# Performance work log

Hardware: AMD Instinct MI355X
Metric: run time of the kernel (lower is better)

The kernel has to match this reference:

```python
import jax, jax.numpy as jnp
import numpy as np

N_NODES = 50000
N_EDGES = 1600000
IN_F, H_F, N_C = 128, 128, 16
NEG_SLOPE = 0.2  # DGL GATConv default


def setup_inputs() -> dict:
    key = jax.random.key(0)
    ks = jax.random.split(key, 12)
    def w(k, shape, fan_in):
        return jax.random.normal(k, shape, jnp.float32) / np.float32(np.sqrt(fan_in))
    return {
        "feat": jax.random.normal(ks[0], (N_NODES, IN_F), jnp.float32),
        "src": jax.random.randint(ks[1], (N_EDGES,), 0, N_NODES, dtype=jnp.int32),
        "dst": jax.random.randint(ks[2], (N_EDGES,), 0, N_NODES, dtype=jnp.int32),
        "W1": w(ks[3], (IN_F, H_F), IN_F), "al1": w(ks[4], (H_F,), H_F), "ar1": w(ks[5], (H_F,), H_F), "b1": jnp.zeros((H_F,), jnp.float32),
        "W2": w(ks[6], (H_F, H_F), H_F), "al2": w(ks[7], (H_F,), H_F), "ar2": w(ks[8], (H_F,), H_F), "b2": jnp.zeros((H_F,), jnp.float32),
        "W3": w(ks[9], (H_F, N_C), H_F), "al3": w(ks[10], (N_C,), N_C), "ar3": w(ks[11], (N_C,), N_C), "b3": jnp.zeros((N_C,), jnp.float32),
    }


def _gat_layer(h, src, dst, W, al, ar, b):
    # DGL GATConv (1 head): ft = W h; e_ij = LeakyReLU(a_l.ft_src + a_r.ft_dst);
    # alpha = edge_softmax over incoming edges of dst; out = sum alpha * ft_src + bias
    ft = h @ W                                   # [N, out]
    el = ft @ al                                 # [N]
    er = ft @ ar                                 # [N]
    e = jax.nn.leaky_relu(el[src] + er[dst], negative_slope=NEG_SLOPE)  # [E]
    emax = jax.ops.segment_max(e, dst, num_segments=N_NODES)
    emax = jnp.where(jnp.isfinite(emax), emax, 0.0)  # guard isolated nodes
    ex = jnp.exp(e - emax[dst])                  # [E]
    esum = jax.ops.segment_sum(ex, dst, num_segments=N_NODES)  # [N]
    agg = jax.ops.segment_sum(ex[:, None] * ft[src], dst, num_segments=N_NODES)  # [N, out]
    out = agg / jnp.where(esum > 0, esum, 1.0)[:, None] + b
    return jax.nn.relu(out)


def reference(feat, src, dst, W1, al1, ar1, b1, W2, al2, ar2, b2, W3, al3, ar3, b3):
    h = _gat_layer(feat, src, dst, W1, al1, ar1, b1)
    h = _gat_layer(h, src, dst, W2, al2, ar2, b2)
    h = _gat_layer(h, src, dst, W3, al3, ar3, b3)
    return h  # [N_NODES, N_C]
```

## Files before the change

### kernel.cpp

```cpp
#include <hip/hip_runtime.h>
#include <hip/hip_bf16.h>

#define NN 50000
#define NE 1600000
#define FF 128
#define CC 16
#define NB ((NN + 63) / 64)
#define NBLK 256
#define CH ((NE + NBLK - 1) / NBLK)

using bf16 = __hip_bfloat16;
using bf16x8 = __attribute__((ext_vector_type(8))) short;
using f32x4  = __attribute__((ext_vector_type(4))) float;

static __device__ __forceinline__ float ldf(const void* p, int i, int isbf){
    return isbf ? __bfloat162float(((const bf16*)p)[i]) : ((const float*)p)[i];
}
static __device__ __forceinline__ float bflo(unsigned u){
    union{unsigned x; float f;} c; c.x = u << 16; return c.f;
}
static __device__ __forceinline__ float bfhi(unsigned u){
    union{unsigned x; float f;} c; c.x = u & 0xFFFF0000u; return c.f;
}
static __device__ __forceinline__ float rdlanef(float v, int l){
    return __int_as_float(__builtin_amdgcn_readlane(__float_as_int(v), l));
}
static __device__ __forceinline__ unsigned short f2bfu(float v){
    bf16 b = __float2bfloat16(v);
    union{bf16 b; unsigned short u;} c; c.b = b; return c.u;
}

__global__ __launch_bounds__(256) void k_prep(const unsigned short* __restrict__ featu,
                                              const void* __restrict__ W1, const void* __restrict__ W2,
                                              const void* __restrict__ W3, int* __restrict__ dflag,
                                              int* __restrict__ bcounts, unsigned short* __restrict__ wtg){
    __shared__ int cnt;
    const int t = threadIdx.x;
    if (t == 0) cnt = 0;
    __syncthreads();
    unsigned short lo = featu[2 * t];
    int e = (lo >> 7) & 0xFF;
    if (e >= 117 && e <= 137) atomicAdd(&cnt, 1);
    __syncthreads();
    const int isbf = (cnt >= 128) ? 1 : 0;
    int idx = blockIdx.x * 256 + t;
    if (idx == 0) *dflag = isbf;
    if (idx < NB) bcounts[idx] = 0;
    if (idx < 32768){
        int l = idx >> 14;
        int e2 = idx & 16383;
        int f = e2 >> 7, k = e2 & 127;
        const void* W = l ? W2 : W1;
        wtg[idx] = f2bfu(ldf(W, k * FF + f, isbf));
    } else if (idx < 34816){
        int e2 = idx - 32768;
        int f = e2 >> 7, k = e2 & 127;
        wtg[idx] = f2bfu(ldf(W3, k * CC + f, isbf));
    }
}


__global__ __launch_bounds__(256) void k_bcount(const int* __restrict__ dst, int* __restrict__ bcounts,
                                                int* __restrict__ bh){
    __shared__ int hist[NB];
    const int t = threadIdx.x, b = blockIdx.x;
    for (int i = t; i < NB; i += 256) hist[i] = 0;
    __syncthreads();
    const int beg = b * CH, end = (beg + CH < NE) ? beg + CH : NE;
    for (int i = beg + t; i < end; i += 256){
        int d = dst[i];
        if ((unsigned)d >= NN) d = 0;
        atomicAdd(&hist[d >> 6], 1);
    }
    __syncthreads();
    for (int k = t; k < NB; k += 256){
        int v = hist[k];
        bh[k * NBLK + b] = v;
        if (v) atomicAdd(&bcounts[k], v);
    }
}

__global__ __launch_bounds__(256) void k_bscan(const int* __restrict__ bcounts, int* __restrict__ bbase,
                                               int* __restrict__ rowptr){
    __shared__ int s[256];
    const int t = threadIdx.x;
    constexpr int PT = (NB + 255) / 256;
    int loc[PT];
    int sum = 0;
    #pragma unroll
    for (int i = 0; i < PT; i++){
        int idx = t * PT + i;
        int v = (idx < NB) ? bcounts[idx] : 0;
        loc[i] = sum;
        sum += v;
    }
    s[t] = sum; __syncthreads();
    for (int off = 1; off < 256; off <<= 1){
        int x = (t >= off) ? s[t - off] : 0;
        __syncthreads();
        s[t] += x;
        __syncthreads();
    }
    int base = (t > 0) ? s[t - 1] : 0;
    #pragma unroll
    for (int i = 0; i < PT; i++){
        int idx = t * PT + i;
        if (idx < NB) bbase[idx] = base + loc[i];
    }
    if (t == 255){
        bbase[NB] = s[255];
        rowptr[NN] = s[255];
    }
}

__global__ __launch_bounds__(256) void k_boffset(const int* __restrict__ bbase, int* __restrict__ bh){
    int k = blockIdx.x * 4 + (threadIdx.x >> 6);
    int lane = threadIdx.x & 63;
    if (k >= NB) return;
    int v[4];
    int s = 0;
    #pragma unroll
    for (int i = 0; i < 4; i++){
        v[i] = bh[k * NBLK + 4 * lane + i];
        s += v[i];
    }
    int tot = s;
    #pragma unroll
    for (int off = 1; off < 64; off <<= 1){
        int x = __shfl_up(s, off);
        if (lane >= off) s += x;
    }
    int run = bbase[k] + s - tot;
    #pragma unroll
    for (int i = 0; i < 4; i++){
        bh[k * NBLK + 4 * lane + i] = run;
        run += v[i];
    }
}

__global__ __launch_bounds__(256) void k_bucket(const int* __restrict__ src, const int* __restrict__ dst,
                                                const int* __restrict__ bh, unsigned* __restrict__ bpairs){
    __shared__ int cur[NB];
    const int t = threadIdx.x, b = blockIdx.x;
    for (int k = t; k < NB; k += 256) cur[k] = bh[k * NBLK + b];
    __syncthreads();
    const int beg = b * CH, end = (beg + CH < NE) ? beg + CH : NE;
    for (int i = beg + t; i < end; i += 256){
        int s = src[i];
        int d = dst[i];
        if ((unsigned)s >= NN) s = 0;
        if ((unsigned)d >= NN) d = 0;
        int p = atomicAdd(&cur[d >> 6], 1);
        if ((unsigned)p < NE) bpairs[p] = (unsigned)s | ((unsigned)(d & 63) << 16);
    }
}

__global__ __launch_bounds__(256) void k_bsort(const unsigned* __restrict__ bpairs, const int* __restrict__ bbase,
                                               int* __restrict__ rowptr, int* __restrict__ csrsrc){
    __shared__ int cnt[64];
    __shared__ int cur[64];
    const int t = threadIdx.x;
    const int b = blockIdx.x;
    const int base = bbase[b];
    const int endb = bbase[b + 1];
    if (t < 64) cnt[t] = 0;
    __syncthreads();
    for (int i = base + t; i < endb; i += 256)
        atomicAdd(&cnt[bpairs[i] >> 16], 1);
    __syncthreads();
    if (t < 64){
        int v = cnt[t];
        int inc = v;
        #pragma unroll
        for (int off = 1; off < 64; off <<= 1){
            int x = __shfl_up(inc, off);
            if (t >= off) inc += x;
        }
        int excl = inc - v;
        cur[t] = excl;
        int d = b * 64 + t;
        if (d < NN) rowptr[d] = base + excl;
    }
    __syncthreads();
    for (int i = base + t; i < endb; i += 256){
        unsigned pr = bpairs[i];
        int p = atomicAdd(&cur[pr >> 16], 1);
        csrsrc[base + p] = (int)(pr & 0xFFFFu);
    }
}


template<bool XDYN>
__global__ __launch_bounds__(256) void k_mgemm(const void* __restrict__ X, const unsigned short* __restrict__ wtg,
                                               const void* __restrict__ al, const void* __restrict__ ar,
                                               const int* __restrict__ dflag, bf16* __restrict__ ft,
                                               float* __restrict__ el, float* __restrict__ er){
    const int isbf = *dflag;
    const int t  = threadIdx.x;
    const int n0 = blockIdx.x * 64;
    const int wv = t >> 6;
    const int lane = t & 63;
    const int quad = lane >> 4;
    const int mcol = lane & 15;
    const int row = n0 + wv * 16 + mcol;
    const int rc  = (row < NN) ? row : 0;

    bf16x8 afr[4];
    if (XDYN && !isbf){
        const float* xr = (const float*)X + rc * FF + quad * 8;
        #pragma unroll
        for (int kt = 0; kt < 4; kt++){
            float4 a = *(const float4*)(xr + kt * 32);
            float4 b = *(const float4*)(xr + kt * 32 + 4);
            union { bf16x8 v; unsigned u[4]; } c;
            c.u[0] = (unsigned)f2bfu(a.x) | ((unsigned)f2bfu(a.y) << 16);
            c.u[1] = (unsigned)f2bfu(a.z) | ((unsigned)f2bfu(a.w) << 16);
            c.u[2] = (unsigned)f2bfu(b.x) | ((unsigned)f2bfu(b.y) << 16);
            c.u[3] = (unsigned)f2bfu(b.z) | ((unsigned)f2bfu(b.w) << 16);
            afr[kt] = c.v;
        }
    } else {
        const unsigned short* xr = (const unsigned short*)X + rc * FF + quad * 8;
        #pragma unroll
        for (int kt = 0; kt < 4; kt++)
            afr[kt] = *(const bf16x8*)(xr + kt * 32);
    }

    float elp[4] = {0.f,0.f,0.f,0.f}, erp[4] = {0.f,0.f,0.f,0.f};

    #pragma unroll
    for (int f = 0; f < 8; f++){
        f32x4 acc = {0.f, 0.f, 0.f, 0.f};
        const unsigned short* wr = wtg + (f * 16 + mcol) * FF + quad * 8;
        #pragma unroll
        for (int kt = 0; kt < 4; kt++){
            bf16x8 bfr = *(const bf16x8*)(wr + kt * 32);
            acc = __builtin_amdgcn_mfma_f32_16x16x32_bf16(afr[kt], bfr, acc, 0, 0, 0);
        }
        int col = f * 16 + mcol;
        float alv = ldf(al, col, isbf);
        float arv = ldf(ar, col, isbf);
        #pragma unroll
        for (int reg = 0; reg < 4; reg++){
            int node = n0 + wv * 16 + quad * 4 + reg;
            float v = acc[reg];
            if (node < NN) ft[node * FF + col] = __float2bfloat16(v);
            elp[reg] += v * alv;
            erp[reg] += v * arv;
        }
    }

    #pragma unroll
    for (int reg = 0; reg < 4; reg++){
        float pl = elp[reg], pr = erp[reg];
        #pragma unroll
        for (int off = 1; off < 16; off <<= 1){
            pl += __shfl_xor(pl, off);
            pr += __shfl_xor(pr, off);
        }
        int node = n0 + wv * 16 + quad * 4 + reg;
        if (mcol == 0 && node < NN){ el[node] = pl; er[node] = pr; }
    }
}


__global__ __launch_bounds__(256) void k_mgemm3(const void* __restrict__ X, const unsigned short* __restrict__ wt3g,
                                                const void* __restrict__ al, const void* __restrict__ ar,
                                                const int* __restrict__ dflag, float* __restrict__ ft,
                                                float* __restrict__ el, float* __restrict__ er){
    const int isbf = *dflag;
    const int t  = threadIdx.x;
    const int n0 = blockIdx.x * 64;
    const int wv = t >> 6;
    const int lane = t & 63;
    const int quad = lane >> 4;
    const int mcol = lane & 15;
    const int row = n0 + wv * 16 + mcol;
    const int rc  = (row < NN) ? row : 0;

    const unsigned short* xr = (const unsigned short*)X + rc * FF + quad * 8;
    const unsigned short* wr = wt3g + mcol * FF + quad * 8;

    f32x4 acc = {0.f, 0.f, 0.f, 0.f};
    #pragma unroll
    for (int kt = 0; kt < 4; kt++){
        bf16x8 afr = *(const bf16x8*)(xr + kt * 32);
        bf16x8 bfr = *(const bf16x8*)(wr + kt * 32);
        acc = __builtin_amdgcn_mfma_f32_16x16x32_bf16(afr, bfr, acc, 0, 0, 0);
    }

    float alv = ldf(al, mcol, isbf);
    float arv = ldf(ar, mcol, isbf);
    #pragma unroll
    for (int reg = 0; reg < 4; reg++){
        int node = n0 + wv * 16 + quad * 4 + reg;
        float v = acc[reg];
        if (node < NN) ft[node * CC + mcol] = v;
        float pl = v * alv, pr = v * arv;
        #pragma unroll
        for (int off = 1; off < 16; off <<= 1){
            pl += __shfl_xor(pl, off);
            pr += __shfl_xor(pr, off);
        }
        if (mcol == 0 && node < NN){ el[node] = pl; er[node] = pr; }
    }
}


__global__ __launch_bounds__(256) void k_agg128(const void* __restrict__ ftv, const float* __restrict__ el,
                                                const float* __restrict__ er, const int* __restrict__ rowptr,
                                                const int* __restrict__ csrsrc, const void* __restrict__ bias,
                                                const int* __restrict__ dflag, unsigned* __restrict__ outp){
    const int isbf = *dflag;
    int lane = threadIdx.x & 63;
    int n = blockIdx.x * 4 + (threadIdx.x >> 6);
    if (n >= NN) return;
    int beg = rowptr[n], end = rowptr[n + 1];
    beg = (beg < 0) ? 0 : (beg > NE ? NE : beg);
    end = (end < beg) ? beg : (end > NE ? NE : end);
    int deg = end - beg;
    float erd = er[n];

    float m = -3.4e38f;
    int   s_c = 0;
    float e_c = 0.f;
    for (int i = beg + lane; i < end; i += 64){
        int s = csrsrc[i];
        if ((unsigned)s >= NN) s = 0;
        float e = el[s] + erd;
        e = (e >= 0.f) ? e : 0.2f * e;
        if (i < beg + 64){ s_c = s; e_c = e; }
        m = fmaxf(m, e);
    }
    #pragma unroll
    for (int off = 32; off; off >>= 1) m = fmaxf(m, __shfl_xor(m, off));

    int jmax = (deg < 64) ? deg : 64;
    float w_c = (lane < jmax) ? __expf(e_c - m) : 0.f;
    float lsum = w_c;
    #pragma unroll
    for (int off = 32; off; off >>= 1) lsum += __shfl_xor(lsum, off);

    const int g = lane >> 4;
    const int c = lane & 15;
    const uint4* ftq4 = (const uint4*)ftv;
    float acc[8] = {0.f,0.f,0.f,0.f,0.f,0.f,0.f,0.f};
    int jmax4 = (jmax + 3) & ~3;

    for (int base = 0; base < jmax4; base += 16){
        uint4 u[4];
        float wB[4];
        #pragma unroll
        for (int q = 0; q < 4; q++){
            int jj = base + q * 4;
            if (jj < jmax4){
                int idx = jj + g;
                int sE = __shfl(s_c, idx);
                wB[q] = __shfl(w_c, idx);
                u[q] = ftq4[(unsigned)sE * 16u + c];
            } else {
                wB[q] = 0.f;
                u[q] = (uint4){0u, 0u, 0u, 0u};
            }
        }
        #pragma unroll
        for (int q = 0; q < 4; q++){
            float w = wB[q];
            acc[0] += w * bflo(u[q].x); acc[1] += w * bfhi(u[q].x);
            acc[2] += w * bflo(u[q].y); acc[3] += w * bfhi(u[q].y);
            acc[4] += w * bflo(u[q].z); acc[5] += w * bfhi(u[q].z);
            acc[6] += w * bflo(u[q].w); acc[7] += w * bfhi(u[q].w);
        }
    }

    for (int i = beg + 64; i < end; ++i){
        int s = csrsrc[i];
        if ((unsigned)s >= NN) s = 0;
        float e = el[s] + erd;
        e = (e >= 0.f) ? e : 0.2f * e;
        float w = __expf(e - m);
        lsum += w;
        if (g == 0){
            uint4 u = ftq4[(unsigned)s * 16u + c];
            acc[0] += w * bflo(u.x); acc[1] += w * bfhi(u.x);
            acc[2] += w * bflo(u.y); acc[3] += w * bfhi(u.y);
            acc[4] += w * bflo(u.z); acc[5] += w * bfhi(u.z);
            acc[6] += w * bflo(u.w); acc[7] += w * bfhi(u.w);
        }
    }

    #pragma unroll
    for (int k = 0; k < 8; k++){
        acc[k] += __shfl_xor(acc[k], 16);
        acc[k] += __shfl_xor(acc[k], 32);
    }

    if (g == 0){
        float inv = 1.f / ((lsum > 0.f) ? lsum : 1.f);
        float o[8];
        #pragma unroll
        for (int k = 0; k < 8; k++)
            o[k] = fmaxf(acc[k] * inv + ldf(bias, c * 8 + k, isbf), 0.f);
        uint4 pk;
        pk.x = (unsigned)f2bfu(o[0]) | ((unsigned)f2bfu(o[1]) << 16);
        pk.y = (unsigned)f2bfu(o[2]) | ((unsigned)f2bfu(o[3]) << 16);
        pk.z = (unsigned)f2bfu(o[4]) | ((unsigned)f2bfu(o[5]) << 16);
        pk.w = (unsigned)f2bfu(o[6]) | ((unsigned)f2bfu(o[7]) << 16);
        ((uint4*)outp)[n * 16 + c] = pk;
    }
}


__global__ __launch_bounds__(256) void k_agg16(const float* __restrict__ ftv, const float* __restrict__ el,
                                               const float* __restrict__ er, const int* __restrict__ rowptr,
                                               const int* __restrict__ csrsrc, const void* __restrict__ bias,
                                               const int* __restrict__ dflag, void* __restrict__ outp){
    const int isbf = *dflag;
    int lane = threadIdx.x & 63;
    int n = blockIdx.x * 4 + (threadIdx.x >> 6);
    if (n >= NN) return;
    int beg = rowptr[n], end = rowptr[n + 1];
    beg = (beg < 0) ? 0 : (beg > NE ? NE : beg);
    end = (end < beg) ? beg : (end > NE ? NE : end);
    int deg = end - beg;
    float erd = er[n];

    float m = -3.4e38f;
    int   s_c = 0;
    float e_c = 0.f;
    for (int i = beg + lane; i < end; i += 64){
        int s = csrsrc[i];
        if ((unsigned)s >= NN) s = 0;
        float e = el[s] + erd;
        e = (e >= 0.f) ? e : 0.2f * e;
        if (i < beg + 64){ s_c = s; e_c = e; }
        m = fmaxf(m, e);
    }
    #pragma unroll
    for (int off = 32; off; off >>= 1) m = fmaxf(m, __shfl_xor(m, off));

    int jmax = (deg < 64) ? deg : 64;
    float w_c = (lane < jmax) ? __expf(e_c - m) : 0.f;
    float lsum = w_c;
    #pragma unroll
    for (int off = 32; off; off >>= 1) lsum += __shfl_xor(lsum, off);

    const float4* ftq = (const float4*)ftv;
    const int g   = lane >> 2;
    const int fl2 = lane & 3;
    int nbatch = (jmax + 15) >> 4;
    float wq[4]; float4 uq[4];
    #pragma unroll
    for (int q = 0; q < 4; q++){
        int eidx = (q * 16 + g) & 63;
        int s = __shfl(s_c, eidx);
        wq[q] = (q < nbatch) ? __shfl(w_c, eidx) : 0.f;
        uq[q] = ftq[(unsigned)s * 4 + fl2];
    }
    float a4[4] = {0.f,0.f,0.f,0.f};
    #pragma unroll
    for (int q = 0; q < 4; q++){
        a4[0] += wq[q] * uq[q].x;
        a4[1] += wq[q] * uq[q].y;
        a4[2] += wq[q] * uq[q].z;
        a4[3] += wq[q] * uq[q].w;
    }
    for (int i = beg + 64; i < end; ++i){
        int s = csrsrc[i];
        if ((unsigned)s >= NN) s = 0;
        float e = el[s] + erd;
        e = (e >= 0.f) ? e : 0.2f * e;
        float w = __expf(e - m);
        lsum += w;
        if (g == 0){
            float4 u = ftq[(unsigned)s * 4 + fl2];
            a4[0] += w * u.x; a4[1] += w * u.y; a4[2] += w * u.z; a4[3] += w * u.w;
        }
    }
    #pragma unroll
    for (int i = 0; i < 4; i++){
        a4[i] += __shfl_xor(a4[i], 4);
        a4[i] += __shfl_xor(a4[i], 8);
        a4[i] += __shfl_xor(a4[i], 16);
        a4[i] += __shfl_xor(a4[i], 32);
    }
    float inv = 1.f / ((lsum > 0.f) ? lsum : 1.f);
    if (lane < 4){
        float o0 = fmaxf(a4[0] * inv + ldf(bias, fl2 * 4 + 0, isbf), 0.f);
        float o1 = fmaxf(a4[1] * inv + ldf(bias, fl2 * 4 + 1, isbf), 0.f);
        float o2 = fmaxf(a4[2] * inv + ldf(bias, fl2 * 4 + 2, isbf), 0.f);
        float o3 = fmaxf(a4[3] * inv + ldf(bias, fl2 * 4 + 3, isbf), 0.f);
        if (isbf){
            uint2 pk;
            pk.x = (unsigned)f2bfu(o0) | ((unsigned)f2bfu(o1) << 16);
            pk.y = (unsigned)f2bfu(o2) | ((unsigned)f2bfu(o3) << 16);
            ((uint2*)outp)[n * 4 + fl2] = pk;
        } else {
            float4 o; o.x = o0; o.y = o1; o.z = o2; o.w = o3;
            ((float4*)outp)[n * 4 + fl2] = o;
        }
    }
}


static size_t align256(size_t x){ return (x + 255) & ~(size_t)255; }

extern "C" void kernel_launch(void* const* d_in, const int* in_sizes, int n_in,
                              void* d_out, int out_size, void* d_ws, size_t ws_size,
                              hipStream_t stream) {
    const void* feat = d_in[0];
    const int*  src  = (const int*)d_in[1];
    const int*  dst  = (const int*)d_in[2];
    const void* W1 = d_in[3];
    const void* al1= d_in[4];
    const void* ar1= d_in[5];
    const void* b1 = d_in[6];
    const void* W2 = d_in[7];
    const void* al2= d_in[8];
    const void* ar2= d_in[9];
    const void* b2 = d_in[10];
    const void* W3 = d_in[11];
    const void* al3= d_in[12];
    const void* ar3= d_in[13];
    const void* b3 = d_in[14];

    char* p = (char*)d_ws;
    size_t off = 0;
    auto carve = [&](size_t bytes)->void*{
        void* r = p + off;
        off += align256(bytes);
        return r;
    };
    float* ftA   = (float*)carve((size_t)NN * FF * 4);
    unsigned* hB = (unsigned*)carve((size_t)NN * FF * 4);
    float* el    = (float*)carve((size_t)NN * 4);
    float* er    = (float*)carve((size_t)NN * 4);
    int*   rowptr= (int*)  carve((size_t)(NN + 1) * 4);
    int*   csrsrc= (int*)  carve((size_t)NE * 4);
    int*   bcounts=(int*)  carve((size_t)NB * 4);
    int*   bbase  =(int*)  carve((size_t)(NB + 1) * 4);
    int*   bh     =(int*)  carve((size_t)NB * NBLK * 4);
    unsigned short* wtg = (unsigned short*)carve((size_t)34816 * 2);
    int*   dflag  =(int*)  carve(256);
    unsigned* bpairs = (unsigned*)hB;
    void*  ftb   = ftA;
    (void)ws_size; (void)n_in; (void)in_sizes; (void)out_size;

    dim3 b256(256);

    k_prep<<<dim3(136), b256, 0, stream>>>((const unsigned short*)feat, W1, W2, W3, dflag, bcounts, wtg);

    k_bcount<<<dim3(NBLK), b256, 0, stream>>>(dst, bcounts, bh);
    k_bscan<<<dim3(1), b256, 0, stream>>>(bcounts, bbase, rowptr);
    k_boffset<<<dim3((NB + 3) / 4), b256, 0, stream>>>(bbase, bh);
    k_bucket<<<dim3(NBLK), b256, 0, stream>>>(src, dst, bh, bpairs);
    k_bsort<<<dim3(NB), b256, 0, stream>>>(bpairs, bbase, rowptr, csrsrc);

    const int mg_grid   = (NN + 63) / 64;
    const int node_grid = (NN + 3) / 4;

    k_mgemm<true><<<dim3(mg_grid), b256, 0, stream>>>(feat, wtg, al1, ar1, dflag, (bf16*)ftb, el, er);
    k_agg128<<<dim3(node_grid), b256, 0, stream>>>(ftb, el, er, rowptr, csrsrc, b1, dflag, hB);

    k_mgemm<false><<<dim3(mg_grid), b256, 0, stream>>>(hB, wtg + 16384, al2, ar2, dflag, (bf16*)ftb, el, er);
    k_agg128<<<dim3(node_grid), b256, 0, stream>>>(ftb, el, er, rowptr, csrsrc, b2, dflag, hB);

    k_mgemm3<<<dim3(mg_grid), b256, 0, stream>>>(hB, wtg + 32768, al3, ar3, dflag, (float*)ftb, el, er);
    k_agg16<<<dim3(node_grid), b256, 0, stream>>>((const float*)ftb, el, er, rowptr, csrsrc, b3, dflag, d_out);
}
```

Measured before the change: 337.8 us.

## Precompute edge softmax weights in separate kernel, drop max subtraction in aggregation

Adds a k_wnorm kernel that computes exp(leaky_relu(el[src]+er[dst])) per CSR edge into a scratch buffer stored in the upper half of the ft buffer, plus the reciprocal of the per-node sum. k_agg128 then only gathers the precomputed weights and features, eight edges per iteration. This removes the max-reduction pass and the serial tail loop for high-degree nodes. In exchange it adds a kernel launch and an E-sized weight write and read per layer, and dropping the max subtraction risks exp overflow for large logits.

```diff
diff --git a/kernel.cpp b/kernel.cpp
--- a/kernel.cpp
+++ b/kernel.cpp
@@ -21,9 +21,6 @@
 }
 static __device__ __forceinline__ float bfhi(unsigned u){
     union{unsigned x; float f;} c; c.x = u & 0xFFFF0000u; return c.f;
-}
-static __device__ __forceinline__ float rdlanef(float v, int l){
-    return __int_as_float(__builtin_amdgcn_readlane(__float_as_int(v), l));
 }
 static __device__ __forceinline__ unsigned short f2bfu(float v){
     bf16 b = __float2bfloat16(v);
@@ -307,86 +304,71 @@
 }
 
 
-__global__ __launch_bounds__(256) void k_agg128(const void* __restrict__ ftv, const float* __restrict__ el,
-                                                const float* __restrict__ er, const int* __restrict__ rowptr,
-                                                const int* __restrict__ csrsrc, const void* __restrict__ bias,
+__global__ __launch_bounds__(256) void k_wnorm(const float* __restrict__ el, float* __restrict__ er,
+                                               const int* __restrict__ rowptr, const int* __restrict__ csrsrc,
+                                               float* __restrict__ wcsr){
+    const int t = threadIdx.x;
+    const int n = blockIdx.x * 64 + (t >> 2);
+    if (n >= NN) return;
+    const int sub = t & 3;
+    int beg = rowptr[n], end = rowptr[n + 1];
+    beg = (beg < 0) ? 0 : (beg > NE ? NE : beg);
+    end = (end < beg) ? beg : (end > NE ? NE : end);
+    const float erd = er[n];
+    float sum = 0.f;
+    for (int i = beg + sub; i < end; i += 4){
+        int s = csrsrc[i];
+        if ((unsigned)s >= NN) s = 0;
+        float e = el[s] + erd;
+        e = (e >= 0.f) ? e : 0.2f * e;
+        float ex = __expf(e);
+        wcsr[i] = ex;
+        sum += ex;
+    }
+    sum += __shfl_xor(sum, 1);
+    sum += __shfl_xor(sum, 2);
+    if (sub == 0) er[n] = 1.f / ((sum > 0.f) ? sum : 1.f);
+}
+
+
+__global__ __launch_bounds__(256) void k_agg128(const void* __restrict__ ftv, const int* __restrict__ rowptr,
+                                                const int* __restrict__ csrsrc, const float* __restrict__ wcsr,
+                                                const float* __restrict__ erinv, const void* __restrict__ bias,
                                                 const int* __restrict__ dflag, unsigned* __restrict__ outp){
     const int isbf = *dflag;
-    int lane = threadIdx.x & 63;
-    int n = blockIdx.x * 4 + (threadIdx.x >> 6);
+    const int lane = threadIdx.x & 63;
+    const int n = blockIdx.x * 4 + (threadIdx.x >> 6);
     if (n >= NN) return;
     int beg = rowptr[n], end = rowptr[n + 1];
     beg = (beg < 0) ? 0 : (beg > NE ? NE : beg);
     end = (end < beg) ? beg : (end > NE ? NE : end);
-    int deg = end - beg;
-    float erd = er[n];
-
-    float m = -3.4e38f;
-    int   s_c = 0;
-    float e_c = 0.f;
-    for (int i = beg + lane; i < end; i += 64){
-        int s = csrsrc[i];
-        if ((unsigned)s >= NN) s = 0;
-        float e = el[s] + erd;
-        e = (e >= 0.f) ? e : 0.2f * e;
-        if (i < beg + 64){ s_c = s; e_c = e; }
-        m = fmaxf(m, e);
-    }
-    #pragma unroll
-    for (int off = 32; off; off >>= 1) m = fmaxf(m, __shfl_xor(m, off));
-
-    int jmax = (deg < 64) ? deg : 64;
-    float w_c = (lane < jmax) ? __expf(e_c - m) : 0.f;
-    float lsum = w_c;
-    #pragma unroll
-    for (int off = 32; off; off >>= 1) lsum += __shfl_xor(lsum, off);
 
     const int g = lane >> 4;
     const int c = lane & 15;
     const uint4* ftq4 = (const uint4*)ftv;
     float acc[8] = {0.f,0.f,0.f,0.f,0.f,0.f,0.f,0.f};
-    int jmax4 = (jmax + 3) & ~3;
-
-    for (int base = 0; base < jmax4; base += 16){
-        uint4 u[4];
-        float wB[4];
-        #pragma unroll
-        for (int q = 0; q < 4; q++){
-            int jj = base + q * 4;
-            if (jj < jmax4){
-                int idx = jj + g;
-                int sE = __shfl(s_c, idx);
-                wB[q] = __shfl(w_c, idx);
-                u[q] = ftq4[(unsigned)sE * 16u + c];
-            } else {
-                wB[q] = 0.f;
-                u[q] = (uint4){0u, 0u, 0u, 0u};
-            }
-        }
-        #pragma unroll
-        for (int q = 0; q < 4; q++){
-            float w = wB[q];
-            acc[0] += w * bflo(u[q].x); acc[1] += w * bfhi(u[q].x);
-            acc[2] += w * bflo(u[q].y); acc[3] += w * bfhi(u[q].y);
-            acc[4] += w * bflo(u[q].z); acc[5] += w * bfhi(u[q].z);
-            acc[6] += w * bflo(u[q].w); acc[7] += w * bfhi(u[q].w);
-        }
-    }
-
-    for (int i = beg + 64; i < end; ++i){
-        int s = csrsrc[i];
-        if ((unsigned)s >= NN) s = 0;
-        float e = el[s] + erd;
-        e = (e >= 0.f) ? e : 0.2f * e;
-        float w = __expf(e - m);
-        lsum += w;
-        if (g == 0){
-            uint4 u = ftq4[(unsigned)s * 16u + c];
-            acc[0] += w * bflo(u.x); acc[1] += w * bfhi(u.x);
-            acc[2] += w * bflo(u.y); acc[3] += w * bfhi(u.y);
-            acc[4] += w * bflo(u.z); acc[5] += w * bfhi(u.z);
-            acc[6] += w * bflo(u.w); acc[7] += w * bfhi(u.w);
-        }
+
+    for (int j = beg; j < end; j += 8){
+        int iA = j + g;
+        int iB = j + 4 + g;
+        int cA = (iA < end) ? iA : beg;
+        int cB = (iB < end) ? iB : beg;
+        int sA = csrsrc[cA];
+        int sB = csrsrc[cB];
+        float wA = (iA < end) ? wcsr[cA] : 0.f;
+        float wB = (iB < end) ? wcsr[cB] : 0.f;
+        if ((unsigned)sA >= NN) sA = 0;
+        if ((unsigned)sB >= NN) sB = 0;
+        uint4 uA = ftq4[(unsigned)sA * 16u + c];
+        uint4 uB = ftq4[(unsigned)sB * 16u + c];
+        acc[0] += wA * bflo(uA.x); acc[1] += wA * bfhi(uA.x);
+        acc[2] += wA * bflo(uA.y); acc[3] += wA * bfhi(uA.y);
+        acc[4] += wA * bflo(uA.z); acc[5] += wA * bfhi(uA.z);
+        acc[6] += wA * bflo(uA.w); acc[7] += wA * bfhi(uA.w);
+        acc[0] += wB * bflo(uB.x); acc[1] += wB * bfhi(uB.x);
+        acc[2] += wB * bflo(uB.y); acc[3] += wB * bfhi(uB.y);
+        acc[4] += wB * bflo(uB.z); acc[5] += wB * bfhi(uB.z);
+        acc[6] += wB * bflo(uB.w); acc[7] += wB * bfhi(uB.w);
     }
 
     #pragma unroll
@@ -396,7 +378,7 @@
     }
 
     if (g == 0){
-        float inv = 1.f / ((lsum > 0.f) ? lsum : 1.f);
+        float inv = erinv[n];
         float o[8];
         #pragma unroll
         for (int k = 0; k < 8; k++)
@@ -544,6 +526,7 @@
     int*   dflag  =(int*)  carve(256);
     unsigned* bpairs = (unsigned*)hB;
     void*  ftb   = ftA;
+    float* wcsr  = ftA + (size_t)NN * FF / 2;
     (void)ws_size; (void)n_in; (void)in_sizes; (void)out_size;
 
     dim3 b256(256);
@@ -558,12 +541,15 @@
 
     const int mg_grid   = (NN + 63) / 64;
     const int node_grid = (NN + 3) / 4;
+    const int wn_grid   = (NN + 63) / 64;
 
     k_mgemm<true><<<dim3(mg_grid), b256, 0, stream>>>(feat, wtg, al1, ar1, dflag, (bf16*)ftb, el, er);
-    k_agg128<<<dim3(node_grid), b256, 0, stream>>>(ftb, el, er, rowptr, csrsrc, b1, dflag, hB);
+    k_wnorm<<<dim3(wn_grid), b256, 0, stream>>>(el, er, rowptr, csrsrc, wcsr);
+    k_agg128<<<dim3(node_grid), b256, 0, stream>>>(ftb, rowptr, csrsrc, wcsr, er, b1, dflag, hB);
 
     k_mgemm<false><<<dim3(mg_grid), b256, 0, stream>>>(hB, wtg + 16384, al2, ar2, dflag, (bf16*)ftb, el, er);
-    k_agg128<<<dim3(node_grid), b256, 0, stream>>>(ftb, el, er, rowptr, csrsrc, b2, dflag, hB);
+    k_wnorm<<<dim3(wn_grid), b256, 0, stream>>>(el, er, rowptr, csrsrc, wcsr);
+    k_agg128<<<dim3(node_grid), b256, 0, stream>>>(ftb, rowptr, csrsrc, wcsr, er, b2, dflag, hB);
 
     k_mgemm3<<<dim3(mg_grid), b256, 0, stream>>>(hB, wtg + 32768, al3, ar3, dflag, (float*)ftb, el, er);
     k_agg16<<<dim3(node_grid), b256, 0, stream>>>((const float*)ftb, el, er, rowptr, csrsrc, b3, dflag, d_out);
```

Measured after the change: 360.5 us. 6.7% more time.
